# Kernel optimization log

Measured on AMD Instinct MI355X. Metric: run time of the kernel, lower is better.

The kernel has to match this reference:

```python
import jax, jax.numpy as jnp
import numpy as np

KP_VARIANCE = 0.01


def make_coordinate_grid(h, w, dtype):
    # Normalized coordinates in [-1, 1], last dim is (x, y) as in monkey-net.
    x = 2.0 * (jnp.arange(w, dtype=dtype) / (w - 1)) - 1.0
    y = 2.0 * (jnp.arange(h, dtype=dtype) / (h - 1)) - 1.0
    xx = jnp.broadcast_to(x[None, :], (h, w))
    yy = jnp.broadcast_to(y[:, None], (h, w))
    return jnp.stack([xx, yy], axis=-1)  # (h, w, 2)


def grid_sample_bilinear(img, grid):
    # img: (N, C, H, W), grid: (N, Hg, Wg, 2) with xy in [-1, 1].
    # Bilinear, align_corners=True, zero padding (torch grid_sample defaults in monkey-net era).
    N, C, H, W = img.shape
    x = (grid[..., 0] + 1.0) * (W - 1) * 0.5
    y = (grid[..., 1] + 1.0) * (H - 1) * 0.5
    x0 = jnp.floor(x); y0 = jnp.floor(y)
    x1 = x0 + 1.0;     y1 = y0 + 1.0
    wx1 = x - x0; wx0 = 1.0 - wx1
    wy1 = y - y0; wy0 = 1.0 - wy1

    def gather(ix, iy):
        valid = ((ix >= 0) & (ix <= W - 1) & (iy >= 0) & (iy <= H - 1)).astype(img.dtype)
        ixc = jnp.clip(ix, 0, W - 1).astype(jnp.int32)
        iyc = jnp.clip(iy, 0, H - 1).astype(jnp.int32)
        vals = jax.vmap(lambda im, yy_, xx_: im[:, yy_, xx_])(img, iyc, ixc)  # (N, C, Hg, Wg)
        return vals * valid[:, None, :, :]

    out = (gather(x0, y0) * (wx0 * wy0)[:, None]
           + gather(x1, y0) * (wx1 * wy0)[:, None]
           + gather(x0, y1) * (wx0 * wy1)[:, None]
           + gather(x1, y1) * (wx1 * wy1)[:, None])
    return out


def setup_inputs() -> dict:
    key = jax.random.key(0)
    k1, k2, k3 = jax.random.split(key, 3)
    bs, c, dsrc, h, w = 4, 3, 1, 128, 128
    d, K = 8, 10
    source_image = jax.random.uniform(k1, (bs, c, dsrc, h, w), jnp.float32)
    kp_driving_mean = jax.random.uniform(k2, (bs, d, K, 2), jnp.float32, minval=-1.0, maxval=1.0)
    kp_source_mean = jax.random.uniform(k3, (bs, d, K, 2), jnp.float32, minval=-1.0, maxval=1.0)
    return {"source_image": source_image,
            "kp_driving_mean": kp_driving_mean,
            "kp_source_mean": kp_source_mean}


def reference(source_image, kp_driving_mean, kp_source_mean):
    bs, c, dsrc, h, w = source_image.shape
    _, d, K, _ = kp_driving_mean.shape
    grid = make_coordinate_grid(h, w, source_image.dtype)  # (h, w, 2)

    # Gaussian heatmaps around driving keypoints: (bs, d, K, h, w)
    diff2 = ((grid - kp_driving_mean[:, :, :, None, None, :]) ** 2).sum(-1)
    heat = jnp.exp(-0.5 * diff2 / KP_VARIANCE)
    heat = heat / heat.sum(axis=(-2, -1), keepdims=True)  # norm_const == 'sum'
    # add background feature map (zeros) as kp index 0
    heat = jnp.concatenate([jnp.zeros((bs, d, 1, h, w), heat.dtype), heat], axis=2)
    K1 = K + 1

    # keypoint motion difference: (bs, d, K1, 2)
    kp_diff = kp_source_mean - kp_driving_mean
    kp_diff = jnp.concatenate([jnp.zeros((bs, d, 1, 2), kp_diff.dtype), kp_diff], axis=2)
    diff_map = jnp.broadcast_to(kp_diff[:, :, :, :, None, None], (bs, d, K1, 2, h, w))

    # deformed source image per (frame, keypoint)
    app = jnp.broadcast_to(source_image[:, None, None], (bs, d, K1, c, dsrc, h, w))
    app = app.reshape(bs * d * K1, c * dsrc, h, w)
    deform = grid[None] + kp_diff.reshape(bs * d * K1, 1, 1, 2)  # (N, h, w, 2)
    deformed = grid_sample_bilinear(app, deform).reshape(bs, d, K1, c * dsrc, h, w)

    enc = jnp.concatenate([heat[:, :, :, None], diff_map, deformed], axis=3)  # (bs,d,K1,1+2+c,h,w)
    enc = enc.reshape(bs, d, -1, h, w)
    enc = jnp.transpose(enc, (0, 2, 1, 3, 4))  # (bs, out_channels, d, h, w)
    return enc
```

## Files before the change

### kernel.cpp

```cpp
#include <hip/hip_runtime.h>
#include <hip/hip_bf16.h>
#include <math.h>

#define BS 4
#define C  3
#define D  8
#define K  10
#define K1 11
#define H  128
#define W  128
#define HW (H*W)

__global__ void memb_norm_kernel(const float* __restrict__ kpd,
                                 float* __restrict__ norm) {
    int idx = blockIdx.x;
    float kx = kpd[idx * 2 + 0];
    float ky = kpd[idx * 2 + 1];
    int lane = threadIdx.x;
    float sx = 0.f, sy = 0.f;
    #pragma unroll
    for (int j = lane; j < W; j += 64) {
        float coord = (float)j * (2.0f / 127.0f) - 1.0f;
        float ddx = coord - kx;
        float ddy = coord - ky;
        sx += __expf(-50.0f * ddx * ddx);
        sy += __expf(-50.0f * ddy * ddy);
    }
    #pragma unroll
    for (int o = 32; o > 0; o >>= 1) {
        sx += __shfl_down(sx, o, 64);
        sy += __shfl_down(sy, o, 64);
    }
    if (lane == 0) norm[idx] = 1.0f / (sx * sy);
}

__global__ void memb_main_kernel(const float* __restrict__ src,
                                 const float* __restrict__ kpd,
                                 const float* __restrict__ kps,
                                 const float* __restrict__ norm,
                                 float* __restrict__ out) {
    int t = blockIdx.x * blockDim.x + threadIdx.x;
    const int total = BS * D * K1 * HW;
    if (t >= total) return;

    int wi = t & (W - 1);
    int hi = (t >> 7) & (H - 1);
    int k  = (t >> 14) % K1;
    int r  = (t >> 14) / K1;
    int di = r & (D - 1);
    int b  = r >> 3;

    float x = (float)wi * (2.0f / 127.0f) - 1.0f;
    float y = (float)hi * (2.0f / 127.0f) - 1.0f;

    float heat = 0.f, dx = 0.f, dy = 0.f;
    if (k > 0) {
        int kidx = r * K + (k - 1);
        float kx  = kpd[kidx * 2 + 0];
        float kyv = kpd[kidx * 2 + 1];
        dx = kps[kidx * 2 + 0] - kx;
        dy = kps[kidx * 2 + 1] - kyv;
        float ex = x - kx, ey = y - kyv;
        heat = __expf(-50.0f * (ex * ex + ey * ey)) * norm[kidx];
    }

    float px = (x + dx + 1.0f) * 63.5f;
    float py = (y + dy + 1.0f) * 63.5f;
    float fx0 = floorf(px), fy0 = floorf(py);
    int x0 = (int)fx0, y0 = (int)fy0;
    int x1 = x0 + 1,   y1 = y0 + 1;
    float wx1 = px - fx0, wy1 = py - fy0;
    float wx0 = 1.0f - wx1, wy0 = 1.0f - wy1;

    float vx0 = (x0 >= 0 && x0 <= W - 1) ? 1.0f : 0.0f;
    float vx1 = (x1 >= 0 && x1 <= W - 1) ? 1.0f : 0.0f;
    float vy0 = (y0 >= 0 && y0 <= H - 1) ? 1.0f : 0.0f;
    float vy1 = (y1 >= 0 && y1 <= H - 1) ? 1.0f : 0.0f;

    int cx0 = min(max(x0, 0), W - 1), cx1 = min(max(x1, 0), W - 1);
    int cy0 = min(max(y0, 0), H - 1), cy1 = min(max(y1, 0), H - 1);

    float w00 = wx0 * wy0 * vx0 * vy0;
    float w10 = wx1 * wy0 * vx1 * vy0;
    float w01 = wx0 * wy1 * vx0 * vy1;
    float w11 = wx1 * wy1 * vx1 * vy1;

    const float* sb = src + (size_t)b * C * HW;
    int o00 = cy0 * W + cx0, o10 = cy0 * W + cx1;
    int o01 = cy1 * W + cx0, o11 = cy1 * W + cx1;

    float v[C];
    #pragma unroll
    for (int ci = 0; ci < C; ci++) {
        const float* sc = sb + ci * HW;
        v[ci] = w00 * sc[o00] + w10 * sc[o10] + w01 * sc[o01] + w11 * sc[o11];
    }

    const size_t cs = (size_t)D * HW;
    size_t base = ((size_t)(b * 66 + k * 6) * D + di) * HW + hi * W + wi;
    out[base + 0 * cs] = heat;
    out[base + 1 * cs] = dx;
    out[base + 2 * cs] = dy;
    out[base + 3 * cs] = v[0];
    out[base + 4 * cs] = v[1];
    out[base + 5 * cs] = v[2];
}

extern "C" void kernel_launch(void* const* d_in, const int* in_sizes, int n_in,
                              void* d_out, int out_size, void* d_ws, size_t ws_size,
                              hipStream_t stream) {
    const float* src = (const float*)d_in[0];
    const float* kpd = (const float*)d_in[1];
    const float* kps = (const float*)d_in[2];
    float* out  = (float*)d_out;
    float* norm = (float*)d_ws;

    memb_norm_kernel<<<BS * D * K, 64, 0, stream>>>(kpd, norm);

    const int total = BS * D * K1 * HW;
    const int block = 256;
    const int grid = (total + block - 1) / block;
    memb_main_kernel<<<grid, block, 0, stream>>>(src, kpd, kps, norm, out);
}
```

Before: 157.3 us.

## Restructure into per-output-plane kernel with separable heatmap and vectorized stores

After: 176.4 us. 1.12x slower.

```diff
diff --git a/kernel.cpp b/kernel.cpp
--- a/kernel.cpp
+++ b/kernel.cpp
@@ -11,99 +11,124 @@
 #define W  128
 #define HW (H*W)
 
-__global__ void memb_norm_kernel(const float* __restrict__ kpd,
-                                 float* __restrict__ norm) {
-    int idx = blockIdx.x;
-    float kx = kpd[idx * 2 + 0];
-    float ky = kpd[idx * 2 + 1];
-    int lane = threadIdx.x;
-    float sx = 0.f, sy = 0.f;
-    #pragma unroll
-    for (int j = lane; j < W; j += 64) {
-        float coord = (float)j * (2.0f / 127.0f) - 1.0f;
-        float ddx = coord - kx;
-        float ddy = coord - ky;
-        sx += __expf(-50.0f * ddx * ddx);
-        sy += __expf(-50.0f * ddy * ddy);
-    }
-    #pragma unroll
-    for (int o = 32; o > 0; o >>= 1) {
-        sx += __shfl_down(sx, o, 64);
-        sy += __shfl_down(sy, o, 64);
-    }
-    if (lane == 0) norm[idx] = 1.0f / (sx * sy);
-}
+__global__ __launch_bounds__(256) void memb_plane_kernel(
+    const float* __restrict__ src,
+    const float* __restrict__ kpd,
+    const float* __restrict__ kps,
+    float* __restrict__ out)
+{
+    const int p   = blockIdx.x;
+    const int b   = p / (66 * D);
+    const int rem = p % (66 * D);
+    const int oc  = rem >> 3;
+    const int di  = rem & (D - 1);
+    const int k   = oc / 6;
+    const int j   = oc % 6;
+    const int tid = threadIdx.x;
 
-__global__ void memb_main_kernel(const float* __restrict__ src,
-                                 const float* __restrict__ kpd,
-                                 const float* __restrict__ kps,
-                                 const float* __restrict__ norm,
-                                 float* __restrict__ out) {
-    int t = blockIdx.x * blockDim.x + threadIdx.x;
-    const int total = BS * D * K1 * HW;
-    if (t >= total) return;
+    float* op = out + (size_t)p * HW;
 
-    int wi = t & (W - 1);
-    int hi = (t >> 7) & (H - 1);
-    int k  = (t >> 14) % K1;
-    int r  = (t >> 14) / K1;
-    int di = r & (D - 1);
-    int b  = r >> 3;
-
-    float x = (float)wi * (2.0f / 127.0f) - 1.0f;
-    float y = (float)hi * (2.0f / 127.0f) - 1.0f;
-
-    float heat = 0.f, dx = 0.f, dy = 0.f;
+    float kx = 0.f, ky = 0.f, dxv = 0.f, dyv = 0.f;
     if (k > 0) {
-        int kidx = r * K + (k - 1);
-        float kx  = kpd[kidx * 2 + 0];
-        float kyv = kpd[kidx * 2 + 1];
-        dx = kps[kidx * 2 + 0] - kx;
-        dy = kps[kidx * 2 + 1] - kyv;
-        float ex = x - kx, ey = y - kyv;
-        heat = __expf(-50.0f * (ex * ex + ey * ey)) * norm[kidx];
+        int kidx = (b * D + di) * K + (k - 1);
+        kx  = kpd[kidx * 2 + 0];
+        ky  = kpd[kidx * 2 + 1];
+        dxv = kps[kidx * 2 + 0] - kx;
+        dyv = kps[kidx * 2 + 1] - ky;
     }
 
-    float px = (x + dx + 1.0f) * 63.5f;
-    float py = (y + dy + 1.0f) * 63.5f;
-    float fx0 = floorf(px), fy0 = floorf(py);
-    int x0 = (int)fx0, y0 = (int)fy0;
-    int x1 = x0 + 1,   y1 = y0 + 1;
-    float wx1 = px - fx0, wy1 = py - fy0;
-    float wx0 = 1.0f - wx1, wy0 = 1.0f - wy1;
-
-    float vx0 = (x0 >= 0 && x0 <= W - 1) ? 1.0f : 0.0f;
-    float vx1 = (x1 >= 0 && x1 <= W - 1) ? 1.0f : 0.0f;
-    float vy0 = (y0 >= 0 && y0 <= H - 1) ? 1.0f : 0.0f;
-    float vy1 = (y1 >= 0 && y1 <= H - 1) ? 1.0f : 0.0f;
-
-    int cx0 = min(max(x0, 0), W - 1), cx1 = min(max(x1, 0), W - 1);
-    int cy0 = min(max(y0, 0), H - 1), cy1 = min(max(y1, 0), H - 1);
-
-    float w00 = wx0 * wy0 * vx0 * vy0;
-    float w10 = wx1 * wy0 * vx1 * vy0;
-    float w01 = wx0 * wy1 * vx0 * vy1;
-    float w11 = wx1 * wy1 * vx1 * vy1;
-
-    const float* sb = src + (size_t)b * C * HW;
-    int o00 = cy0 * W + cx0, o10 = cy0 * W + cx1;
-    int o01 = cy1 * W + cx0, o11 = cy1 * W + cx1;
-
-    float v[C];
-    #pragma unroll
-    for (int ci = 0; ci < C; ci++) {
-        const float* sc = sb + ci * HW;
-        v[ci] = w00 * sc[o00] + w10 * sc[o10] + w01 * sc[o01] + w11 * sc[o11];
+    if (j == 1 || j == 2) {
+        float val = (j == 1) ? dxv : dyv;
+        float4 v4 = make_float4(val, val, val, val);
+        #pragma unroll
+        for (int it = 0; it < 16; it++)
+            ((float4*)op)[it * 256 + tid] = v4;
+        return;
     }
 
-    const size_t cs = (size_t)D * HW;
-    size_t base = ((size_t)(b * 66 + k * 6) * D + di) * HW + hi * W + wi;
-    out[base + 0 * cs] = heat;
-    out[base + 1 * cs] = dx;
-    out[base + 2 * cs] = dy;
-    out[base + 3 * cs] = v[0];
-    out[base + 4 * cs] = v[1];
-    out[base + 5 * cs] = v[2];
+    if (j == 0) {
+        if (k == 0) {
+            float4 z = make_float4(0.f, 0.f, 0.f, 0.f);
+            #pragma unroll
+            for (int it = 0; it < 16; it++)
+                ((float4*)op)[it * 256 + tid] = z;
+            return;
+        }
+        __shared__ float gx[128], gy[128], red[2];
+        if (tid < 128) {
+            float c = (float)tid * (2.0f / 127.0f) - 1.0f - kx;
+            gx[tid] = __expf(-50.0f * c * c);
+        } else {
+            int i = tid - 128;
+            float c = (float)i * (2.0f / 127.0f) - 1.0f - ky;
+            gy[i] = __expf(-50.0f * c * c);
+        }
+        __syncthreads();
+        if (tid < 64) {
+            float v = gx[tid] + gx[tid + 64];
+            #pragma unroll
+            for (int o = 32; o > 0; o >>= 1) v += __shfl_down(v, o, 64);
+            if (tid == 0) red[0] = v;
+        } else if (tid < 128) {
+            int l = tid - 64;
+            float v = gy[l] + gy[l + 64];
+            #pragma unroll
+            for (int o = 32; o > 0; o >>= 1) v += __shfl_down(v, o, 64);
+            if (l == 0) red[1] = v;
+        }
+        __syncthreads();
+        float nrm = 1.0f / (red[0] * red[1]);
+        #pragma unroll 4
+        for (int it = 0; it < 16; it++) {
+            int ch = it * 256 + tid;
+            int hi = ch >> 5;
+            int wi = (ch & 31) << 2;
+            float g = nrm * gy[hi];
+            float4 gxv = *(const float4*)(gx + wi);
+            ((float4*)op)[ch] = make_float4(g * gxv.x, g * gxv.y,
+                                            g * gxv.z, g * gxv.w);
+        }
+        return;
+    }
+
+    const int ci = j - 3;
+    float ox = dxv * 63.5f;
+    float oy = dyv * 63.5f;
+    float fox = floorf(ox), foy = floorf(oy);
+    int bcol = (int)fox, arow = (int)foy;
+    float wx1 = ox - fox, wx0 = 1.0f - wx1;
+    float wy1 = oy - foy, wy0 = 1.0f - wy1;
+    const float* sp = src + ((size_t)b * C + ci) * HW;
+
+    #pragma unroll 4
+    for (int it = 0; it < 16; it++) {
+        int ch = it * 256 + tid;
+        int hi = ch >> 5;
+        int wi = (ch & 31) << 2;
+        int y0 = hi + arow, y1 = y0 + 1;
+        int col0 = wi + bcol;
+        float vy0 = (y0 >= 0 && y0 < H) ? wy0 : 0.0f;
+        float vy1 = (y1 >= 0 && y1 < H) ? wy1 : 0.0f;
+        int cy0 = min(max(y0, 0), H - 1);
+        int cy1 = min(max(y1, 0), H - 1);
+        const float* r0 = sp + cy0 * W;
+        const float* r1 = sp + cy1 * W;
+        float s0[5], s1[5];
+        #pragma unroll
+        for (int e = 0; e < 5; e++) {
+            int c = col0 + e;
+            float vm = (c >= 0 && c < W) ? 1.0f : 0.0f;
+            int cc = min(max(c, 0), W - 1);
+            s0[e] = r0[cc] * vm;
+            s1[e] = r1[cc] * vm;
+        }
+        float4 o4;
+        o4.x = vy0 * (wx0 * s0[0] + wx1 * s0[1]) + vy1 * (wx0 * s1[0] + wx1 * s1[1]);
+        o4.y = vy0 * (wx0 * s0[1] + wx1 * s0[2]) + vy1 * (wx0 * s1[1] + wx1 * s1[2]);
+        o4.z = vy0 * (wx0 * s0[2] + wx1 * s0[3]) + vy1 * (wx0 * s1[2] + wx1 * s1[3]);
+        o4.w = vy0 * (wx0 * s0[3] + wx1 * s0[4]) + vy1 * (wx0 * s1[3] + wx1 * s1[4]);
+        ((float4*)op)[ch] = o4;
+    }
 }
 
 extern "C" void kernel_launch(void* const* d_in, const int* in_sizes, int n_in,
@@ -112,13 +137,8 @@
     const float* src = (const float*)d_in[0];
     const float* kpd = (const float*)d_in[1];
     const float* kps = (const float*)d_in[2];
-    float* out  = (float*)d_out;
-    float* norm = (float*)d_ws;
+    float* out = (float*)d_out;
 
-    memb_norm_kernel<<<BS * D * K, 64, 0, stream>>>(kpd, norm);
-
-    const int total = BS * D * K1 * HW;
-    const int block = 256;
-    const int grid = (total + block - 1) / block;
-    memb_main_kernel<<<grid, block, 0, stream>>>(src, kpd, kps, norm, out);
+    const int planes = BS * 66 * D;
+    memb_plane_kernel<<<planes, 256, 0, stream>>>(src, kpd, kps, out);
 }
```
